# Performance work log

Measured on AMD Instinct MI355X. Metric: run time of the kernel, lower is better.

## Reference

```python
import jax, jax.numpy as jnp
import numpy as np

# Tsit5 Butcher tableau (Tsitouras 2011), 5th-order solution weights.
C2, C3, C4, C5 = 0.161, 0.327, 0.9, 0.9800255409045097
A21 = 0.161
A31, A32 = -0.008480655492356989, 0.335480655492357
A41, A42, A43 = 2.8971530571054935, -6.359448489975075, 4.3622954328695815
A51, A52, A53, A54 = 5.325864828439257, -11.748883564062828, 7.4955393428898365, -0.09249506636175525
A61, A62, A63, A64, A65 = 5.86145544294642, -12.92096931784711, 8.159367898576159, -0.071584973281401, -0.028269050394068383
B1, B2, B3, B4, B5, B6 = 0.09646076681806523, 0.01, 0.4798896504144996, 1.379008574103742, -3.290069515436081, 2.324710524099774


def setup_inputs() -> dict:
    key = jax.random.key(0)
    k0, k1, k2, k3 = jax.random.split(key, 4)
    B, D, W, T = 2048, 64, 128, 50
    y0 = jax.random.normal(k0, (B, D), dtype=jnp.float32)
    ts = (jnp.arange(T, dtype=jnp.float32)) * 0.02  # t0=0, t1=0.98, dt0=0.02
    # equinox-style MLP params (Linear stores weight as [out, in]); scaled for stability
    w0 = jax.random.normal(k1, (W, D + 1), dtype=jnp.float32) / np.sqrt(D + 1)
    b0 = jnp.zeros((W,), dtype=jnp.float32)
    w1 = jax.random.normal(k2, (W, W), dtype=jnp.float32) / np.sqrt(W)
    b1 = jnp.zeros((W,), dtype=jnp.float32)
    w2 = jax.random.normal(k3, (D, W), dtype=jnp.float32) / np.sqrt(W)
    b2 = jnp.zeros((D,), dtype=jnp.float32)
    return {"y0": y0, "ts": ts, "w0": w0, "b0": b0, "w1": w1, "b1": b1, "w2": w2, "b2": b2}


def reference(y0, ts, w0, b0, w1, b1, w2, b2):
    # dynamics f(t, y) = MLP(concat([t, y])), vectorized over batch
    def dyn(t, y):
        tcol = jnp.full((y.shape[0], 1), t, dtype=y.dtype)
        inp = jnp.concatenate([tcol, y], axis=1)           # [B, D+1]
        h = jax.nn.relu(inp @ w0.T + b0)                    # [B, W]
        h = jax.nn.relu(h @ w1.T + b1)                      # [B, W]
        return h @ w2.T + b2                                # [B, D]

    dt = ts[1] - ts[0]

    def step(y, t):
        k1 = dyn(t, y)
        k2 = dyn(t + C2 * dt, y + dt * (A21 * k1))
        k3 = dyn(t + C3 * dt, y + dt * (A31 * k1 + A32 * k2))
        k4 = dyn(t + C4 * dt, y + dt * (A41 * k1 + A42 * k2 + A43 * k3))
        k5 = dyn(t + C5 * dt, y + dt * (A51 * k1 + A52 * k2 + A53 * k3 + A54 * k4))
        k6 = dyn(t + dt, y + dt * (A61 * k1 + A62 * k2 + A63 * k3 + A64 * k4 + A65 * k5))
        y_new = y + dt * (B1 * k1 + B2 * k2 + B3 * k3 + B4 * k4 + B5 * k5 + B6 * k6)
        return y_new, None

    yT, _ = jax.lax.scan(step, y0, ts[:-1])  # 49 constant-size Tsit5 steps
    return yT
```

## Files before the change

kernel.cpp:

```cpp
#include <hip/hip_runtime.h>

typedef __attribute__((ext_vector_type(8))) short   short8;
typedef __attribute__((ext_vector_type(8))) __bf16  bf16x8;
typedef __attribute__((ext_vector_type(4))) __bf16  bf16x4;
typedef __attribute__((ext_vector_type(4))) float   f32x4;
typedef __attribute__((ext_vector_type(4))) unsigned short ushort4v;

#define NSTEPS 49

static __device__ __forceinline__ short8 as_s8(bf16x8 v) {
    return __builtin_bit_cast(short8, v);
}
static __device__ __forceinline__ bf16x4 pack4(f32x4 v) {
    bf16x4 b;
    b[0] = (__bf16)v[0]; b[1] = (__bf16)v[1];
    b[2] = (__bf16)v[2]; b[3] = (__bf16)v[3];
    return b;
}

#define MFMA(A, B, C) __builtin_amdgcn_mfma_f32_16x16x32_bf16((A), (B), (C), 0, 0, 0)

#define BUILD_XT(TV)                                                         \
    {                                                                        \
        bf16x8 v_;                                                           \
        _Pragma("unroll") for (int j_ = 0; j_ < 8; ++j_) v_[j_] = (__bf16)0.f; \
        if (q == 0) { v_[0] = (__bf16)(TV); v_[1] = (__bf16)1.0f; }          \
        xt = as_s8(v_);                                                      \
    }

#define RELU_PACK(AA, AB, OUT)                                               \
    {                                                                        \
        bf16x8 v_;                                                           \
        v_[0]=(__bf16)fmaxf((AA)[0],0.f); v_[1]=(__bf16)fmaxf((AA)[1],0.f);  \
        v_[2]=(__bf16)fmaxf((AA)[2],0.f); v_[3]=(__bf16)fmaxf((AA)[3],0.f);  \
        v_[4]=(__bf16)fmaxf((AB)[0],0.f); v_[5]=(__bf16)fmaxf((AB)[1],0.f);  \
        v_[6]=(__bf16)fmaxf((AB)[2],0.f); v_[7]=(__bf16)fmaxf((AB)[3],0.f);  \
        OUT = as_s8(v_);                                                     \
    }

#define STAGE(TN, HS)                                                        \
    {                                                                        \
        const f32x4 zz = {0.f, 0.f, 0.f, 0.f};                               \
                             \
        short8 xs0 = *(const short8*)(&XS[0][lane][0]);                      \
        short8 xs1 = *(const short8*)(&XS[1][lane][0]);                      \
        short8 xt; BUILD_XT(TN);                                             \
        f32x4 aA = MFMA(wL1[0], xs0, zz); aA = MFMA(wL1[1], xs1, aA);        \
        aA = MFMA(wL1[2], xt, aA);                                           \
        f32x4 aB = MFMA(wL1[3], xs0, zz); aB = MFMA(wL1[4], xs1, aB);        \
        aB = MFMA(wL1[5], xt, aB);                                           \
        short8 xhm; RELU_PACK(aA, aB, xhm);                                  \
        *(short8*)(&XH[w][lane][0]) = xhm;                                   \
        __syncthreads();                                                     \
                              \
        short8 xh0 = *(const short8*)(&XH[0][lane][0]);                      \
        short8 xh1 = *(const short8*)(&XH[1][lane][0]);                      \
        short8 xh2 = *(const short8*)(&XH[2][lane][0]);                      \
        short8 xh3 = *(const short8*)(&XH[3][lane][0]);                      \
        f32x4 gA = MFMA(wL2[0], xh0, bL2v[0]); gA = MFMA(wL2[1], xh1, gA);   \
        gA = MFMA(wL2[2], xh2, gA);            gA = MFMA(wL2[3], xh3, gA);   \
        f32x4 gB = MFMA(wL2[4], xh0, bL2v[1]); gB = MFMA(wL2[5], xh1, gB);   \
        gB = MFMA(wL2[6], xh2, gB);            gB = MFMA(wL2[7], xh3, gB);   \
        short8 xgm; RELU_PACK(gA, gB, xgm);                                  \
        *(short8*)(&XG[w][lane][0]) = xgm;                                   \
        __syncthreads();                                                     \
                    \
        short8 xg0 = *(const short8*)(&XG[0][lane][0]);                      \
        short8 xg1 = *(const short8*)(&XG[1][lane][0]);                      \
        short8 xg2 = *(const short8*)(&XG[2][lane][0]);                      \
        short8 xg3 = *(const short8*)(&XG[3][lane][0]);                      \
        kv = MFMA(wL3[0], xg0, bL3v); kv = MFMA(wL3[1], xg1, kv);            \
        kv = MFMA(wL3[2], xg2, kv);   kv = MFMA(wL3[3], xg3, kv);            \
        _Pragma("unroll")                                                    \
        for (int r_ = 0; r_ < 4; ++r_) si[r_] = pre[r_] + (HS) * kv[r_];     \
        *(ushort4v*)(&XS[w >> 1][lane][4 * (w & 1)]) =                       \
            __builtin_bit_cast(ushort4v, pack4(si));                        \
        __syncthreads();                                                     \
    }

extern "C" __global__ void __launch_bounds__(256, 1)
node_solve(const float* __restrict__ y0, const float* __restrict__ ts,
           const float* __restrict__ gw0, const float* __restrict__ gb0,
           const float* __restrict__ gw1, const float* __restrict__ gb1,
           const float* __restrict__ gw2, const float* __restrict__ gb2,
           float* __restrict__ out)
{
    __shared__ __align__(16) unsigned short XS[2][64][8];
    __shared__ __align__(16) unsigned short XH[4][64][8];
    __shared__ __align__(16) unsigned short XG[4][64][8];

    const int tid  = threadIdx.x;
    const int w    = tid >> 6;
    const int lane = tid & 63;
    const int q    = lane >> 4;
    const int c    = lane & 15;
    const int row0 = blockIdx.x << 4;

    short8 wL1[6];
    short8 wL2[8];
    short8 wL3[4];
    f32x4  bL2v[2], bL3v;

    #pragma unroll
    for (int p = 0; p < 2; ++p) {
        const int t = 2 * w + p;
        const int n = 16 * t + c;
        const float* w0r = gw0 + n * 65 + 1;
        #pragma unroll
        for (int ks = 0; ks < 2; ++ks) {
            bf16x8 v;
            #pragma unroll
            for (int j = 0; j < 8; ++j)
                v[j] = (__bf16)w0r[32*ks + 16*(j>>2) + 4*q + (j&3)];
            wL1[3*p + ks] = as_s8(v);
        }
        {
            bf16x8 v;
            #pragma unroll
            for (int j = 0; j < 8; ++j) v[j] = (__bf16)0.f;
            if (q == 0) { v[0] = (__bf16)gw0[n*65]; v[1] = (__bf16)gb0[n]; }
            wL1[3*p + 2] = as_s8(v);
        }
        const float* w1r = gw1 + n * 128;
        #pragma unroll
        for (int ks = 0; ks < 4; ++ks) {
            bf16x8 v;
            #pragma unroll
            for (int j = 0; j < 8; ++j)
                v[j] = (__bf16)w1r[32*ks + 16*(j>>2) + 4*q + (j&3)];
            wL2[4*p + ks] = as_s8(v);
        }
        bL2v[p] = *(const f32x4*)(gb1 + 16*t + 4*q);
    }
    {
        const int n = 16 * w + c;
        const float* w2r = gw2 + n * 128;
        #pragma unroll
        for (int ks = 0; ks < 4; ++ks) {
            bf16x8 v;
            #pragma unroll
            for (int j = 0; j < 8; ++j)
                v[j] = (__bf16)w2r[32*ks + 16*(j>>2) + 4*q + (j&3)];
            wL3[ks] = as_s8(v);
        }
        bL3v = *(const f32x4*)(gb2 + 16*w + 4*q);
    }

    f32x4 yn = *(const f32x4*)(y0 + (size_t)(row0 + c) * 64 + 16*w + 4*q);

    const float ts0 = ts[0];
    const float dtv = ts[1] - ts[0];

    const float e1 = dtv * 0.09646076681806523f, e2 = dtv * 0.01f;
    const float e3 = dtv * 0.4798896504144996f,  e4 = dtv * 1.379008574103742f;
    const float e5 = dtv * -3.290069515436081f,  e6 = dtv * 2.324710524099774f;
    const float h0 = dtv * 0.161f;
    const float h1 = dtv * 0.335480655492357f;
    const float h2 = dtv * 4.3622954328695815f;
    const float h3 = dtv * -0.09249506636175525f;
    const float h4 = dtv * -0.028269050394068383f;
    const float g31 = dtv * (-0.008480655492356989f - 0.09646076681806523f);
    const float g41 = dtv * (2.8971530571054935f    - 0.09646076681806523f);
    const float g42 = dtv * (-6.359448489975075f    - 0.01f);
    const float g51 = dtv * (5.325864828439257f     - 0.09646076681806523f);
    const float g52 = dtv * (-11.748883564062828f   - 0.01f);
    const float g53 = dtv * (7.4955393428898365f    - 0.4798896504144996f);
    const float g61 = dtv * (5.86145544294642f      - 0.09646076681806523f);
    const float g62 = dtv * (-12.92096931784711f    - 0.01f);
    const float g63 = dtv * (8.159367898576159f     - 0.4798896504144996f);
    const float g64 = dtv * (-0.071584973281401f    - 1.379008574103742f);

    *(ushort4v*)(&XS[w >> 1][lane][4 * (w & 1)]) =
        __builtin_bit_cast(ushort4v, pack4(yn));
    f32x4 pre = yn, si, kv;
    __syncthreads();

    #pragma unroll 1
    for (int step = 0; step < NSTEPS; ++step) {
        const float t0s = ts0 + (float)step * dtv;
        bf16x4 kb0, kb1, kb2, kb3;

        STAGE(t0s, h0)
        #pragma unroll
        for (int r = 0; r < 4; ++r) yn[r] += e1 * kv[r];
        kb0 = pack4(kv);
        #pragma unroll
        for (int r = 0; r < 4; ++r) pre[r] = yn[r] + g31 * (float)kb0[r];

        STAGE(t0s + 0.161f * dtv, h1)
        #pragma unroll
        for (int r = 0; r < 4; ++r) yn[r] += e2 * kv[r];
        kb1 = pack4(kv);
        #pragma unroll
        for (int r = 0; r < 4; ++r)
            pre[r] = yn[r] + g41 * (float)kb0[r] + g42 * (float)kb1[r];

        STAGE(t0s + 0.327f * dtv, h2)
        #pragma unroll
        for (int r = 0; r < 4; ++r) yn[r] += e3 * kv[r];
        kb2 = pack4(kv);
        #pragma unroll
        for (int r = 0; r < 4; ++r)
            pre[r] = yn[r] + g51 * (float)kb0[r] + g52 * (float)kb1[r]
                   + g53 * (float)kb2[r];

        STAGE(t0s + 0.9f * dtv, h3)
        #pragma unroll
        for (int r = 0; r < 4; ++r) yn[r] += e4 * kv[r];
        kb3 = pack4(kv);
        #pragma unroll
        for (int r = 0; r < 4; ++r)
            pre[r] = yn[r] + g61 * (float)kb0[r] + g62 * (float)kb1[r]
                   + g63 * (float)kb2[r] + g64 * (float)kb3[r];

        STAGE(t0s + 0.9800255409045097f * dtv, h4)
        #pragma unroll
        for (int r = 0; r < 4; ++r) { yn[r] += e5 * kv[r]; pre[r] = yn[r]; }

        STAGE(t0s + dtv, e6)
        #pragma unroll
        for (int r = 0; r < 4; ++r) { yn[r] = si[r]; pre[r] = si[r]; }
    }

    *(f32x4*)(&out[(size_t)(row0 + c) * 64 + 16*w + 4*q]) = yn;
}

extern "C" void kernel_launch(void* const* d_in, const int* in_sizes, int n_in,
                              void* d_out, int out_size, void* d_ws, size_t ws_size,
                              hipStream_t stream) {
    const float* y0 = (const float*)d_in[0];
    const float* ts = (const float*)d_in[1];
    const float* w0 = (const float*)d_in[2];
    const float* b0 = (const float*)d_in[3];
    const float* w1 = (const float*)d_in[4];
    const float* b1 = (const float*)d_in[5];
    const float* w2 = (const float*)d_in[6];
    const float* b2 = (const float*)d_in[7];
    float* out = (float*)d_out;

    node_solve<<<dim3(128), dim3(256), 0, stream>>>(y0, ts, w0, b0, w1, b1, w2, b2, out);
}
```

Before: 244.4 us.

## Process two 16-row batch tiles per block to interleave MFMA chains

Each block now handles 32 batch rows as two independent 16-row tiles, duplicating the shared-memory staging buffers and interleaving both tiles' MFMA chains within each stage. The intent is to hide MFMA and LDS latency in this serial, latency-bound solver and to amortize barriers and register-resident weights over more rows. In exchange the grid halves to 64 blocks, leaving more compute units idle, and register pressure per thread rises.

```diff
diff --git a/kernel.cpp b/kernel.cpp
--- a/kernel.cpp
+++ b/kernel.cpp
@@ -38,43 +38,72 @@
         OUT = as_s8(v_);                                                     \
     }
 
-#define STAGE(TN, HS)                                                        \
+#define STAGE2(TN, HS)                                                       \
     {                                                                        \
         const f32x4 zz = {0.f, 0.f, 0.f, 0.f};                               \
-                             \
-        short8 xs0 = *(const short8*)(&XS[0][lane][0]);                      \
-        short8 xs1 = *(const short8*)(&XS[1][lane][0]);                      \
         short8 xt; BUILD_XT(TN);                                             \
-        f32x4 aA = MFMA(wL1[0], xs0, zz); aA = MFMA(wL1[1], xs1, aA);        \
-        aA = MFMA(wL1[2], xt, aA);                                           \
-        f32x4 aB = MFMA(wL1[3], xs0, zz); aB = MFMA(wL1[4], xs1, aB);        \
-        aB = MFMA(wL1[5], xt, aB);                                           \
-        short8 xhm; RELU_PACK(aA, aB, xhm);                                  \
-        *(short8*)(&XH[w][lane][0]) = xhm;                                   \
+                 \
+        short8 xs0A = *(const short8*)(&XSA[0][lane][0]);                    \
+        short8 xs1A = *(const short8*)(&XSA[1][lane][0]);                    \
+        short8 xs0B = *(const short8*)(&XSB[0][lane][0]);                    \
+        short8 xs1B = *(const short8*)(&XSB[1][lane][0]);                    \
+        f32x4 hAa = MFMA(wL1[0], xs0A, zz); hAa = MFMA(wL1[1], xs1A, hAa);   \
+        hAa = MFMA(wL1[2], xt, hAa);                                         \
+        f32x4 hAb = MFMA(wL1[3], xs0A, zz); hAb = MFMA(wL1[4], xs1A, hAb);   \
+        hAb = MFMA(wL1[5], xt, hAb);                                         \
+        f32x4 hBa = MFMA(wL1[0], xs0B, zz); hBa = MFMA(wL1[1], xs1B, hBa);   \
+        hBa = MFMA(wL1[2], xt, hBa);                                         \
+        f32x4 hBb = MFMA(wL1[3], xs0B, zz); hBb = MFMA(wL1[4], xs1B, hBb);   \
+        hBb = MFMA(wL1[5], xt, hBb);                                         \
+        short8 xhmA; RELU_PACK(hAa, hAb, xhmA);                              \
+        short8 xhmB; RELU_PACK(hBa, hBb, xhmB);                              \
+        *(short8*)(&XHA[w][lane][0]) = xhmA;                                 \
+        *(short8*)(&XHB[w][lane][0]) = xhmB;                                 \
         __syncthreads();                                                     \
-                              \
-        short8 xh0 = *(const short8*)(&XH[0][lane][0]);                      \
-        short8 xh1 = *(const short8*)(&XH[1][lane][0]);                      \
-        short8 xh2 = *(const short8*)(&XH[2][lane][0]);                      \
-        short8 xh3 = *(const short8*)(&XH[3][lane][0]);                      \
-        f32x4 gA = MFMA(wL2[0], xh0, bL2v[0]); gA = MFMA(wL2[1], xh1, gA);   \
-        gA = MFMA(wL2[2], xh2, gA);            gA = MFMA(wL2[3], xh3, gA);   \
-        f32x4 gB = MFMA(wL2[4], xh0, bL2v[1]); gB = MFMA(wL2[5], xh1, gB);   \
-        gB = MFMA(wL2[6], xh2, gB);            gB = MFMA(wL2[7], xh3, gB);   \
-        short8 xgm; RELU_PACK(gA, gB, xgm);                                  \
-        *(short8*)(&XG[w][lane][0]) = xgm;                                   \
+                                              \
+        short8 xh0A = *(const short8*)(&XHA[0][lane][0]);                    \
+        short8 xh1A = *(const short8*)(&XHA[1][lane][0]);                    \
+        short8 xh2A = *(const short8*)(&XHA[2][lane][0]);                    \
+        short8 xh3A = *(const short8*)(&XHA[3][lane][0]);                    \
+        short8 xh0B = *(const short8*)(&XHB[0][lane][0]);                    \
+        short8 xh1B = *(const short8*)(&XHB[1][lane][0]);                    \
+        short8 xh2B = *(const short8*)(&XHB[2][lane][0]);                    \
+        short8 xh3B = *(const short8*)(&XHB[3][lane][0]);                    \
+        f32x4 gAa = MFMA(wL2[0], xh0A, bL2v[0]); gAa = MFMA(wL2[1], xh1A, gAa); \
+        gAa = MFMA(wL2[2], xh2A, gAa);           gAa = MFMA(wL2[3], xh3A, gAa); \
+        f32x4 gAb = MFMA(wL2[4], xh0A, bL2v[1]); gAb = MFMA(wL2[5], xh1A, gAb); \
+        gAb = MFMA(wL2[6], xh2A, gAb);           gAb = MFMA(wL2[7], xh3A, gAb); \
+        f32x4 gBa = MFMA(wL2[0], xh0B, bL2v[0]); gBa = MFMA(wL2[1], xh1B, gBa); \
+        gBa = MFMA(wL2[2], xh2B, gBa);           gBa = MFMA(wL2[3], xh3B, gBa); \
+        f32x4 gBb = MFMA(wL2[4], xh0B, bL2v[1]); gBb = MFMA(wL2[5], xh1B, gBb); \
+        gBb = MFMA(wL2[6], xh2B, gBb);           gBb = MFMA(wL2[7], xh3B, gBb); \
+        short8 xgmA; RELU_PACK(gAa, gAb, xgmA);                              \
+        short8 xgmB; RELU_PACK(gBa, gBb, xgmB);                              \
+        *(short8*)(&XGA[w][lane][0]) = xgmA;                                 \
+        *(short8*)(&XGB[w][lane][0]) = xgmB;                                 \
         __syncthreads();                                                     \
-                    \
-        short8 xg0 = *(const short8*)(&XG[0][lane][0]);                      \
-        short8 xg1 = *(const short8*)(&XG[1][lane][0]);                      \
-        short8 xg2 = *(const short8*)(&XG[2][lane][0]);                      \
-        short8 xg3 = *(const short8*)(&XG[3][lane][0]);                      \
-        kv = MFMA(wL3[0], xg0, bL3v); kv = MFMA(wL3[1], xg1, kv);            \
-        kv = MFMA(wL3[2], xg2, kv);   kv = MFMA(wL3[3], xg3, kv);            \
+                            \
+        short8 xg0A = *(const short8*)(&XGA[0][lane][0]);                    \
+        short8 xg1A = *(const short8*)(&XGA[1][lane][0]);                    \
+        short8 xg2A = *(const short8*)(&XGA[2][lane][0]);                    \
+        short8 xg3A = *(const short8*)(&XGA[3][lane][0]);                    \
+        short8 xg0B = *(const short8*)(&XGB[0][lane][0]);                    \
+        short8 xg1B = *(const short8*)(&XGB[1][lane][0]);                    \
+        short8 xg2B = *(const short8*)(&XGB[2][lane][0]);                    \
+        short8 xg3B = *(const short8*)(&XGB[3][lane][0]);                    \
+        kvA = MFMA(wL3[0], xg0A, bL3v); kvA = MFMA(wL3[1], xg1A, kvA);       \
+        kvA = MFMA(wL3[2], xg2A, kvA);  kvA = MFMA(wL3[3], xg3A, kvA);       \
+        kvB = MFMA(wL3[0], xg0B, bL3v); kvB = MFMA(wL3[1], xg1B, kvB);       \
+        kvB = MFMA(wL3[2], xg2B, kvB);  kvB = MFMA(wL3[3], xg3B, kvB);       \
         _Pragma("unroll")                                                    \
-        for (int r_ = 0; r_ < 4; ++r_) si[r_] = pre[r_] + (HS) * kv[r_];     \
-        *(ushort4v*)(&XS[w >> 1][lane][4 * (w & 1)]) =                       \
-            __builtin_bit_cast(ushort4v, pack4(si));                        \
+        for (int r_ = 0; r_ < 4; ++r_) {                                     \
+            siA[r_] = preA[r_] + (HS) * kvA[r_];                             \
+            siB[r_] = preB[r_] + (HS) * kvB[r_];                             \
+        }                                                                    \
+        *(ushort4v*)(&XSA[w >> 1][lane][4 * (w & 1)]) =                      \
+            __builtin_bit_cast(ushort4v, pack4(siA));                       \
+        *(ushort4v*)(&XSB[w >> 1][lane][4 * (w & 1)]) =                      \
+            __builtin_bit_cast(ushort4v, pack4(siB));                       \
         __syncthreads();                                                     \
     }
 
@@ -85,16 +114,16 @@
            const float* __restrict__ gw2, const float* __restrict__ gb2,
            float* __restrict__ out)
 {
-    __shared__ __align__(16) unsigned short XS[2][64][8];
-    __shared__ __align__(16) unsigned short XH[4][64][8];
-    __shared__ __align__(16) unsigned short XG[4][64][8];
+    __shared__ __align__(16) unsigned short XSA[2][64][8], XSB[2][64][8];
+    __shared__ __align__(16) unsigned short XHA[4][64][8], XHB[4][64][8];
+    __shared__ __align__(16) unsigned short XGA[4][64][8], XGB[4][64][8];
 
     const int tid  = threadIdx.x;
     const int w    = tid >> 6;
     const int lane = tid & 63;
     const int q    = lane >> 4;
     const int c    = lane & 15;
-    const int row0 = blockIdx.x << 4;
+    const int row0 = blockIdx.x << 5;
 
     short8 wL1[6];
     short8 wL2[8];
@@ -146,7 +175,8 @@
         bL3v = *(const f32x4*)(gb2 + 16*w + 4*q);
     }
 
-    f32x4 yn = *(const f32x4*)(y0 + (size_t)(row0 + c) * 64 + 16*w + 4*q);
+    f32x4 ynA = *(const f32x4*)(y0 + (size_t)(row0 + c)      * 64 + 16*w + 4*q);
+    f32x4 ynB = *(const f32x4*)(y0 + (size_t)(row0 + 16 + c) * 64 + 16*w + 4*q);
 
     const float ts0 = ts[0];
     const float dtv = ts[1] - ts[0];
@@ -170,59 +200,79 @@
     const float g63 = dtv * (8.159367898576159f     - 0.4798896504144996f);
     const float g64 = dtv * (-0.071584973281401f    - 1.379008574103742f);
 
-    *(ushort4v*)(&XS[w >> 1][lane][4 * (w & 1)]) =
-        __builtin_bit_cast(ushort4v, pack4(yn));
-    f32x4 pre = yn, si, kv;
+    *(ushort4v*)(&XSA[w >> 1][lane][4 * (w & 1)]) =
+        __builtin_bit_cast(ushort4v, pack4(ynA));
+    *(ushort4v*)(&XSB[w >> 1][lane][4 * (w & 1)]) =
+        __builtin_bit_cast(ushort4v, pack4(ynB));
+    f32x4 preA = ynA, preB = ynB, siA, siB, kvA, kvB;
     __syncthreads();
 
     #pragma unroll 1
     for (int step = 0; step < NSTEPS; ++step) {
         const float t0s = ts0 + (float)step * dtv;
-        bf16x4 kb0, kb1, kb2, kb3;
-
-        STAGE(t0s, h0)
-        #pragma unroll
-        for (int r = 0; r < 4; ++r) yn[r] += e1 * kv[r];
-        kb0 = pack4(kv);
-        #pragma unroll
-        for (int r = 0; r < 4; ++r) pre[r] = yn[r] + g31 * (float)kb0[r];
-
-        STAGE(t0s + 0.161f * dtv, h1)
-        #pragma unroll
-        for (int r = 0; r < 4; ++r) yn[r] += e2 * kv[r];
-        kb1 = pack4(kv);
-        #pragma unroll
-        for (int r = 0; r < 4; ++r)
-            pre[r] = yn[r] + g41 * (float)kb0[r] + g42 * (float)kb1[r];
-
-        STAGE(t0s + 0.327f * dtv, h2)
-        #pragma unroll
-        for (int r = 0; r < 4; ++r) yn[r] += e3 * kv[r];
-        kb2 = pack4(kv);
-        #pragma unroll
-        for (int r = 0; r < 4; ++r)
-            pre[r] = yn[r] + g51 * (float)kb0[r] + g52 * (float)kb1[r]
-                   + g53 * (float)kb2[r];
-
-        STAGE(t0s + 0.9f * dtv, h3)
-        #pragma unroll
-        for (int r = 0; r < 4; ++r) yn[r] += e4 * kv[r];
-        kb3 = pack4(kv);
-        #pragma unroll
-        for (int r = 0; r < 4; ++r)
-            pre[r] = yn[r] + g61 * (float)kb0[r] + g62 * (float)kb1[r]
-                   + g63 * (float)kb2[r] + g64 * (float)kb3[r];
-
-        STAGE(t0s + 0.9800255409045097f * dtv, h4)
-        #pragma unroll
-        for (int r = 0; r < 4; ++r) { yn[r] += e5 * kv[r]; pre[r] = yn[r]; }
-
-        STAGE(t0s + dtv, e6)
-        #pragma unroll
-        for (int r = 0; r < 4; ++r) { yn[r] = si[r]; pre[r] = si[r]; }
-    }
-
-    *(f32x4*)(&out[(size_t)(row0 + c) * 64 + 16*w + 4*q]) = yn;
+        bf16x4 kA0, kA1, kA2, kA3, kB0, kB1, kB2, kB3;
+
+        STAGE2(t0s, h0)
+        #pragma unroll
+        for (int r = 0; r < 4; ++r) { ynA[r] += e1 * kvA[r]; ynB[r] += e1 * kvB[r]; }
+        kA0 = pack4(kvA); kB0 = pack4(kvB);
+        #pragma unroll
+        for (int r = 0; r < 4; ++r) {
+            preA[r] = ynA[r] + g31 * (float)kA0[r];
+            preB[r] = ynB[r] + g31 * (float)kB0[r];
+        }
+
+        STAGE2(t0s + 0.161f * dtv, h1)
+        #pragma unroll
+        for (int r = 0; r < 4; ++r) { ynA[r] += e2 * kvA[r]; ynB[r] += e2 * kvB[r]; }
+        kA1 = pack4(kvA); kB1 = pack4(kvB);
+        #pragma unroll
+        for (int r = 0; r < 4; ++r) {
+            preA[r] = ynA[r] + g41 * (float)kA0[r] + g42 * (float)kA1[r];
+            preB[r] = ynB[r] + g41 * (float)kB0[r] + g42 * (float)kB1[r];
+        }
+
+        STAGE2(t0s + 0.327f * dtv, h2)
+        #pragma unroll
+        for (int r = 0; r < 4; ++r) { ynA[r] += e3 * kvA[r]; ynB[r] += e3 * kvB[r]; }
+        kA2 = pack4(kvA); kB2 = pack4(kvB);
+        #pragma unroll
+        for (int r = 0; r < 4; ++r) {
+            preA[r] = ynA[r] + g51 * (float)kA0[r] + g52 * (float)kA1[r]
+                    + g53 * (float)kA2[r];
+            preB[r] = ynB[r] + g51 * (float)kB0[r] + g52 * (float)kB1[r]
+                    + g53 * (float)kB2[r];
+        }
+
+        STAGE2(t0s + 0.9f * dtv, h3)
+        #pragma unroll
+        for (int r = 0; r < 4; ++r) { ynA[r] += e4 * kvA[r]; ynB[r] += e4 * kvB[r]; }
+        kA3 = pack4(kvA); kB3 = pack4(kvB);
+        #pragma unroll
+        for (int r = 0; r < 4; ++r) {
+            preA[r] = ynA[r] + g61 * (float)kA0[r] + g62 * (float)kA1[r]
+                    + g63 * (float)kA2[r] + g64 * (float)kA3[r];
+            preB[r] = ynB[r] + g61 * (float)kB0[r] + g62 * (float)kB1[r]
+                    + g63 * (float)kB2[r] + g64 * (float)kB3[r];
+        }
+
+        STAGE2(t0s + 0.9800255409045097f * dtv, h4)
+        #pragma unroll
+        for (int r = 0; r < 4; ++r) {
+            ynA[r] += e5 * kvA[r]; preA[r] = ynA[r];
+            ynB[r] += e5 * kvB[r]; preB[r] = ynB[r];
+        }
+
+        STAGE2(t0s + dtv, e6)
+        #pragma unroll
+        for (int r = 0; r < 4; ++r) {
+            ynA[r] = siA[r]; preA[r] = siA[r];
+            ynB[r] = siB[r]; preB[r] = siB[r];
+        }
+    }
+
+    *(f32x4*)(&out[(size_t)(row0 + c)      * 64 + 16*w + 4*q]) = ynA;
+    *(f32x4*)(&out[(size_t)(row0 + 16 + c) * 64 + 16*w + 4*q]) = ynB;
 }
 
 extern "C" void kernel_launch(void* const* d_in, const int* in_sizes, int n_in,
@@ -238,5 +288,5 @@
     const float* b2 = (const float*)d_in[7];
     float* out = (float*)d_out;
 
-    node_solve<<<dim3(128), dim3(256), 0, stream>>>(y0, ts, w0, b0, w1, b1, w2, b2, out);
-}
+    node_solve<<<dim3(64), dim3(256), 0, stream>>>(y0, ts, w0, b0, w1, b1, w2, b2, out);
+}
```

Result: slower. 345.5 us (+41.4%).

## Compute full layer-3 output redundantly per wave to drop state LDS exchange

Applied to the files above, without the earlier changes.

Each wave now computes all four 16-column tiles of the final layer instead of one, so every wave holds the full stage output in registers. The next stage's input fragments are built directly from those registers, which removes the XS shared buffer and one __syncthreads per stage. In exchange, layer-3 MFMA work is quadrupled per wave, register use grows (16 weight fragments, four-way state arrays), and the elementwise Runge-Kutta updates are replicated across waves.

```diff
diff --git a/kernel.cpp b/kernel.cpp
--- a/kernel.cpp
+++ b/kernel.cpp
@@ -2,23 +2,26 @@
 
 typedef __attribute__((ext_vector_type(8))) short   short8;
 typedef __attribute__((ext_vector_type(8))) __bf16  bf16x8;
-typedef __attribute__((ext_vector_type(4))) __bf16  bf16x4;
 typedef __attribute__((ext_vector_type(4))) float   f32x4;
-typedef __attribute__((ext_vector_type(4))) unsigned short ushort4v;
 
 #define NSTEPS 49
 
 static __device__ __forceinline__ short8 as_s8(bf16x8 v) {
     return __builtin_bit_cast(short8, v);
 }
-static __device__ __forceinline__ bf16x4 pack4(f32x4 v) {
-    bf16x4 b;
-    b[0] = (__bf16)v[0]; b[1] = (__bf16)v[1];
-    b[2] = (__bf16)v[2]; b[3] = (__bf16)v[3];
-    return b;
-}
 
 #define MFMA(A, B, C) __builtin_amdgcn_mfma_f32_16x16x32_bf16((A), (B), (C), 0, 0, 0)
+
+#define BUILD_XS(SRC)                                                        \
+    {                                                                        \
+        bf16x8 v0_, v1_;                                                     \
+        _Pragma("unroll")                                                    \
+        for (int j_ = 0; j_ < 8; ++j_) {                                     \
+            v0_[j_] = (__bf16)(SRC)[j_ >> 2][j_ & 3];                        \
+            v1_[j_] = (__bf16)(SRC)[(j_ >> 2) + 2][j_ & 3];                  \
+        }                                                                    \
+        xs0 = as_s8(v0_); xs1 = as_s8(v1_);                                  \
+    }
 
 #define BUILD_XT(TV)                                                         \
     {                                                                        \
@@ -27,6 +30,18 @@
         if (q == 0) { v_[0] = (__bf16)(TV); v_[1] = (__bf16)1.0f; }          \
         xt = as_s8(v_);                                                      \
     }
+
+#define STORE_KB(KB, KV)                                                     \
+    {                                                                        \
+        bf16x8 t0_, t1_;                                                     \
+        _Pragma("unroll")                                                    \
+        for (int j_ = 0; j_ < 8; ++j_) {                                     \
+            t0_[j_] = (__bf16)(KV)[j_ >> 2][j_ & 3];                         \
+            t1_[j_] = (__bf16)(KV)[(j_ >> 2) + 2][j_ & 3];                   \
+        }                                                                    \
+        (KB)[0] = t0_; (KB)[1] = t1_;                                        \
+    }
+#define KF(KB, V) ((float)(KB)[(V) >> 3][(V) & 7])
 
 #define RELU_PACK(AA, AB, OUT)                                               \
     {                                                                        \
@@ -41,10 +56,8 @@
 #define STAGE(TN, HS)                                                        \
     {                                                                        \
         const f32x4 zz = {0.f, 0.f, 0.f, 0.f};                               \
-                             \
-        short8 xs0 = *(const short8*)(&XS[0][lane][0]);                      \
-        short8 xs1 = *(const short8*)(&XS[1][lane][0]);                      \
         short8 xt; BUILD_XT(TN);                                             \
+                   \
         f32x4 aA = MFMA(wL1[0], xs0, zz); aA = MFMA(wL1[1], xs1, aA);        \
         aA = MFMA(wL1[2], xt, aA);                                           \
         f32x4 aB = MFMA(wL1[3], xs0, zz); aB = MFMA(wL1[4], xs1, aB);        \
@@ -52,7 +65,7 @@
         short8 xhm; RELU_PACK(aA, aB, xhm);                                  \
         *(short8*)(&XH[w][lane][0]) = xhm;                                   \
         __syncthreads();                                                     \
-                              \
+                                             \
         short8 xh0 = *(const short8*)(&XH[0][lane][0]);                      \
         short8 xh1 = *(const short8*)(&XH[1][lane][0]);                      \
         short8 xh2 = *(const short8*)(&XH[2][lane][0]);                      \
@@ -64,18 +77,25 @@
         short8 xgm; RELU_PACK(gA, gB, xgm);                                  \
         *(short8*)(&XG[w][lane][0]) = xgm;                                   \
         __syncthreads();                                                     \
-                    \
+                        \
         short8 xg0 = *(const short8*)(&XG[0][lane][0]);                      \
         short8 xg1 = *(const short8*)(&XG[1][lane][0]);                      \
         short8 xg2 = *(const short8*)(&XG[2][lane][0]);                      \
         short8 xg3 = *(const short8*)(&XG[3][lane][0]);                      \
-        kv = MFMA(wL3[0], xg0, bL3v); kv = MFMA(wL3[1], xg1, kv);            \
-        kv = MFMA(wL3[2], xg2, kv);   kv = MFMA(wL3[3], xg3, kv);            \
-        _Pragma("unroll")                                                    \
-        for (int r_ = 0; r_ < 4; ++r_) si[r_] = pre[r_] + (HS) * kv[r_];     \
-        *(ushort4v*)(&XS[w >> 1][lane][4 * (w & 1)]) =                       \
-            __builtin_bit_cast(ushort4v, pack4(si));                        \
-        __syncthreads();                                                     \
+        _Pragma("unroll")                                                    \
+        for (int t_ = 0; t_ < 4; ++t_) {                                     \
+            f32x4 ac_ = MFMA(wL3[4*t_ + 0], xg0, bL3v[t_]);                  \
+            ac_ = MFMA(wL3[4*t_ + 1], xg1, ac_);                             \
+            ac_ = MFMA(wL3[4*t_ + 2], xg2, ac_);                             \
+            ac_ = MFMA(wL3[4*t_ + 3], xg3, ac_);                             \
+            kv[t_] = ac_;                                                    \
+        }                                                                    \
+        f32x4 si_[4];                                                        \
+        _Pragma("unroll")                                                    \
+        for (int t_ = 0; t_ < 4; ++t_) si_[t_] = pre[t_] + (HS) * kv[t_];    \
+        BUILD_XS(si_);                                                       \
+        lastsi0 = si_[0]; lastsi1 = si_[1];                                  \
+        lastsi2 = si_[2]; lastsi3 = si_[3];                                  \
     }
 
 extern "C" __global__ void __launch_bounds__(256, 1)
@@ -85,7 +105,6 @@
            const float* __restrict__ gw2, const float* __restrict__ gb2,
            float* __restrict__ out)
 {
-    __shared__ __align__(16) unsigned short XS[2][64][8];
     __shared__ __align__(16) unsigned short XH[4][64][8];
     __shared__ __align__(16) unsigned short XG[4][64][8];
 
@@ -98,8 +117,8 @@
 
     short8 wL1[6];
     short8 wL2[8];
-    short8 wL3[4];
-    f32x4  bL2v[2], bL3v;
+    short8 wL3[16];
+    f32x4  bL2v[2], bL3v[4];
 
     #pragma unroll
     for (int p = 0; p < 2; ++p) {
@@ -132,8 +151,9 @@
         }
         bL2v[p] = *(const f32x4*)(gb1 + 16*t + 4*q);
     }
-    {
-        const int n = 16 * w + c;
+    #pragma unroll
+    for (int t = 0; t < 4; ++t) {
+        const int n = 16 * t + c;
         const float* w2r = gw2 + n * 128;
         #pragma unroll
         for (int ks = 0; ks < 4; ++ks) {
@@ -141,12 +161,15 @@
             #pragma unroll
             for (int j = 0; j < 8; ++j)
                 v[j] = (__bf16)w2r[32*ks + 16*(j>>2) + 4*q + (j&3)];
-            wL3[ks] = as_s8(v);
-        }
-        bL3v = *(const f32x4*)(gb2 + 16*w + 4*q);
-    }
-
-    f32x4 yn = *(const f32x4*)(y0 + (size_t)(row0 + c) * 64 + 16*w + 4*q);
+            wL3[4*t + ks] = as_s8(v);
+        }
+        bL3v[t] = *(const f32x4*)(gb2 + 16*t + 4*q);
+    }
+
+    f32x4 yn[4];
+    #pragma unroll
+    for (int t = 0; t < 4; ++t)
+        yn[t] = *(const f32x4*)(y0 + (size_t)(row0 + c) * 64 + 16*t + 4*q);
 
     const float ts0 = ts[0];
     const float dtv = ts[1] - ts[0];
@@ -170,59 +193,64 @@
     const float g63 = dtv * (8.159367898576159f     - 0.4798896504144996f);
     const float g64 = dtv * (-0.071584973281401f    - 1.379008574103742f);
 
-    *(ushort4v*)(&XS[w >> 1][lane][4 * (w & 1)]) =
-        __builtin_bit_cast(ushort4v, pack4(yn));
-    f32x4 pre = yn, si, kv;
-    __syncthreads();
+    short8 xs0, xs1;
+    f32x4  pre[4], kv[4];
+    f32x4  lastsi0, lastsi1, lastsi2, lastsi3;
+
+    BUILD_XS(yn);
+    #pragma unroll
+    for (int t = 0; t < 4; ++t) pre[t] = yn[t];
 
     #pragma unroll 1
     for (int step = 0; step < NSTEPS; ++step) {
         const float t0s = ts0 + (float)step * dtv;
-        bf16x4 kb0, kb1, kb2, kb3;
+        bf16x8 kb0[2], kb1[2], kb2[2], kb3[2];
 
         STAGE(t0s, h0)
         #pragma unroll
-        for (int r = 0; r < 4; ++r) yn[r] += e1 * kv[r];
-        kb0 = pack4(kv);
-        #pragma unroll
-        for (int r = 0; r < 4; ++r) pre[r] = yn[r] + g31 * (float)kb0[r];
+        for (int t = 0; t < 4; ++t) yn[t] += e1 * kv[t];
+        STORE_KB(kb0, kv);
+        #pragma unroll
+        for (int v = 0; v < 16; ++v)
+            pre[v>>2][v&3] = yn[v>>2][v&3] + g31 * KF(kb0, v);
 
         STAGE(t0s + 0.161f * dtv, h1)
         #pragma unroll
-        for (int r = 0; r < 4; ++r) yn[r] += e2 * kv[r];
-        kb1 = pack4(kv);
-        #pragma unroll
-        for (int r = 0; r < 4; ++r)
-            pre[r] = yn[r] + g41 * (float)kb0[r] + g42 * (float)kb1[r];
+        for (int t = 0; t < 4; ++t) yn[t] += e2 * kv[t];
+        STORE_KB(kb1, kv);
+        #pragma unroll
+        for (int v = 0; v < 16; ++v)
+            pre[v>>2][v&3] = yn[v>>2][v&3] + g41*KF(kb0,v) + g42*KF(kb1,v);
 
         STAGE(t0s + 0.327f * dtv, h2)
         #pragma unroll
-        for (int r = 0; r < 4; ++r) yn[r] += e3 * kv[r];
-        kb2 = pack4(kv);
-        #pragma unroll
-        for (int r = 0; r < 4; ++r)
-            pre[r] = yn[r] + g51 * (float)kb0[r] + g52 * (float)kb1[r]
-                   + g53 * (float)kb2[r];
+        for (int t = 0; t < 4; ++t) yn[t] += e3 * kv[t];
+        STORE_KB(kb2, kv);
+        #pragma unroll
+        for (int v = 0; v < 16; ++v)
+            pre[v>>2][v&3] = yn[v>>2][v&3] + g51*KF(kb0,v) + g52*KF(kb1,v)
+                           + g53*KF(kb2,v);
 
         STAGE(t0s + 0.9f * dtv, h3)
         #pragma unroll
-        for (int r = 0; r < 4; ++r) yn[r] += e4 * kv[r];
-        kb3 = pack4(kv);
-        #pragma unroll
-        for (int r = 0; r < 4; ++r)
-            pre[r] = yn[r] + g61 * (float)kb0[r] + g62 * (float)kb1[r]
-                   + g63 * (float)kb2[r] + g64 * (float)kb3[r];
+        for (int t = 0; t < 4; ++t) yn[t] += e4 * kv[t];
+        STORE_KB(kb3, kv);
+        #pragma unroll
+        for (int v = 0; v < 16; ++v)
+            pre[v>>2][v&3] = yn[v>>2][v&3] + g61*KF(kb0,v) + g62*KF(kb1,v)
+                           + g63*KF(kb2,v) + g64*KF(kb3,v);
 
         STAGE(t0s + 0.9800255409045097f * dtv, h4)
         #pragma unroll
-        for (int r = 0; r < 4; ++r) { yn[r] += e5 * kv[r]; pre[r] = yn[r]; }
+        for (int t = 0; t < 4; ++t) { yn[t] += e5 * kv[t]; pre[t] = yn[t]; }
 
         STAGE(t0s + dtv, e6)
-        #pragma unroll
-        for (int r = 0; r < 4; ++r) { yn[r] = si[r]; pre[r] = si[r]; }
-    }
-
-    *(f32x4*)(&out[(size_t)(row0 + c) * 64 + 16*w + 4*q]) = yn;
+        yn[0] = lastsi0; yn[1] = lastsi1; yn[2] = lastsi2; yn[3] = lastsi3;
+        #pragma unroll
+        for (int t = 0; t < 4; ++t) pre[t] = yn[t];
+    }
+
+    *(f32x4*)(&out[(size_t)(row0 + c) * 64 + 16*w + 4*q]) = yn[w];
 }
 
 extern "C" void kernel_launch(void* const* d_in, const int* in_sizes, int n_in,
```

Measured after the change: 277.4 us. +13.5%, slower.

## Compute full first layer redundantly per wave to drop one barrier per stage

Applied to the files above, without the earlier changes.

Each wave now holds all 24 first-layer weight fragments and computes the whole 128-wide hidden layer itself instead of a quarter slice, removing the XH shared buffer and one __syncthreads per stage. The state reads from shared memory move to the end of each stage. This spends four times the first-layer MFMA work and many more weight registers per wave in exchange for fewer barriers on a latency-bound serial chain.

```diff
diff --git a/kernel.cpp b/kernel.cpp
--- a/kernel.cpp
+++ b/kernel.cpp
@@ -41,30 +41,28 @@
 #define STAGE(TN, HS)                                                        \
     {                                                                        \
         const f32x4 zz = {0.f, 0.f, 0.f, 0.f};                               \
-                             \
-        short8 xs0 = *(const short8*)(&XS[0][lane][0]);                      \
-        short8 xs1 = *(const short8*)(&XS[1][lane][0]);                      \
         short8 xt; BUILD_XT(TN);                                             \
-        f32x4 aA = MFMA(wL1[0], xs0, zz); aA = MFMA(wL1[1], xs1, aA);        \
-        aA = MFMA(wL1[2], xt, aA);                                           \
-        f32x4 aB = MFMA(wL1[3], xs0, zz); aB = MFMA(wL1[4], xs1, aB);        \
-        aB = MFMA(wL1[5], xt, aB);                                           \
-        short8 xhm; RELU_PACK(aA, aB, xhm);                                  \
-        *(short8*)(&XH[w][lane][0]) = xhm;                                   \
-        __syncthreads();                                                     \
-                              \
-        short8 xh0 = *(const short8*)(&XH[0][lane][0]);                      \
-        short8 xh1 = *(const short8*)(&XH[1][lane][0]);                      \
-        short8 xh2 = *(const short8*)(&XH[2][lane][0]);                      \
-        short8 xh3 = *(const short8*)(&XH[3][lane][0]);                      \
-        f32x4 gA = MFMA(wL2[0], xh0, bL2v[0]); gA = MFMA(wL2[1], xh1, gA);   \
-        gA = MFMA(wL2[2], xh2, gA);            gA = MFMA(wL2[3], xh3, gA);   \
-        f32x4 gB = MFMA(wL2[4], xh0, bL2v[1]); gB = MFMA(wL2[5], xh1, gB);   \
-        gB = MFMA(wL2[6], xh2, gB);            gB = MFMA(wL2[7], xh3, gB);   \
+         \
+        short8 xh_[4];                                                       \
+        _Pragma("unroll")                                                    \
+        for (int p_ = 0; p_ < 4; ++p_) {                                     \
+            f32x4 aA_ = MFMA(wL1a[6*p_ + 0], xs0, zz);                       \
+            aA_ = MFMA(wL1a[6*p_ + 1], xs1, aA_);                            \
+            aA_ = MFMA(wL1a[6*p_ + 2], xt,  aA_);                            \
+            f32x4 aB_ = MFMA(wL1a[6*p_ + 3], xs0, zz);                       \
+            aB_ = MFMA(wL1a[6*p_ + 4], xs1, aB_);                            \
+            aB_ = MFMA(wL1a[6*p_ + 5], xt,  aB_);                            \
+            RELU_PACK(aA_, aB_, xh_[p_]);                                    \
+        }                                                                    \
+           \
+        f32x4 gA = MFMA(wL2[0], xh_[0], bL2v[0]); gA = MFMA(wL2[1], xh_[1], gA); \
+        gA = MFMA(wL2[2], xh_[2], gA);            gA = MFMA(wL2[3], xh_[3], gA); \
+        f32x4 gB = MFMA(wL2[4], xh_[0], bL2v[1]); gB = MFMA(wL2[5], xh_[1], gB); \
+        gB = MFMA(wL2[6], xh_[2], gB);            gB = MFMA(wL2[7], xh_[3], gB); \
         short8 xgm; RELU_PACK(gA, gB, xgm);                                  \
         *(short8*)(&XG[w][lane][0]) = xgm;                                   \
         __syncthreads();                                                     \
-                    \
+              \
         short8 xg0 = *(const short8*)(&XG[0][lane][0]);                      \
         short8 xg1 = *(const short8*)(&XG[1][lane][0]);                      \
         short8 xg2 = *(const short8*)(&XG[2][lane][0]);                      \
@@ -76,6 +74,9 @@
         *(ushort4v*)(&XS[w >> 1][lane][4 * (w & 1)]) =                       \
             __builtin_bit_cast(ushort4v, pack4(si));                        \
         __syncthreads();                                                     \
+            \
+        xs0 = *(const short8*)(&XS[0][lane][0]);                             \
+        xs1 = *(const short8*)(&XS[1][lane][0]);                             \
     }
 
 extern "C" __global__ void __launch_bounds__(256, 1)
@@ -86,7 +87,6 @@
            float* __restrict__ out)
 {
     __shared__ __align__(16) unsigned short XS[2][64][8];
-    __shared__ __align__(16) unsigned short XH[4][64][8];
     __shared__ __align__(16) unsigned short XG[4][64][8];
 
     const int tid  = threadIdx.x;
@@ -96,31 +96,35 @@
     const int c    = lane & 15;
     const int row0 = blockIdx.x << 4;
 
-    short8 wL1[6];
+    short8 wL1a[24];
     short8 wL2[8];
     short8 wL3[4];
     f32x4  bL2v[2], bL3v;
 
+    #pragma unroll
+    for (int t = 0; t < 8; ++t) {
+        const int n = 16 * t + c;
+        const float* w0r = gw0 + n * 65 + 1;
+        #pragma unroll
+        for (int ks = 0; ks < 2; ++ks) {
+            bf16x8 v;
+            #pragma unroll
+            for (int j = 0; j < 8; ++j)
+                v[j] = (__bf16)w0r[32*ks + 16*(j>>2) + 4*q + (j&3)];
+            wL1a[3*t + ks] = as_s8(v);
+        }
+        {
+            bf16x8 v;
+            #pragma unroll
+            for (int j = 0; j < 8; ++j) v[j] = (__bf16)0.f;
+            if (q == 0) { v[0] = (__bf16)gw0[n*65]; v[1] = (__bf16)gb0[n]; }
+            wL1a[3*t + 2] = as_s8(v);
+        }
+    }
     #pragma unroll
     for (int p = 0; p < 2; ++p) {
         const int t = 2 * w + p;
         const int n = 16 * t + c;
-        const float* w0r = gw0 + n * 65 + 1;
-        #pragma unroll
-        for (int ks = 0; ks < 2; ++ks) {
-            bf16x8 v;
-            #pragma unroll
-            for (int j = 0; j < 8; ++j)
-                v[j] = (__bf16)w0r[32*ks + 16*(j>>2) + 4*q + (j&3)];
-            wL1[3*p + ks] = as_s8(v);
-        }
-        {
-            bf16x8 v;
-            #pragma unroll
-            for (int j = 0; j < 8; ++j) v[j] = (__bf16)0.f;
-            if (q == 0) { v[0] = (__bf16)gw0[n*65]; v[1] = (__bf16)gb0[n]; }
-            wL1[3*p + 2] = as_s8(v);
-        }
         const float* w1r = gw1 + n * 128;
         #pragma unroll
         for (int ks = 0; ks < 4; ++ks) {
@@ -174,6 +178,8 @@
         __builtin_bit_cast(ushort4v, pack4(yn));
     f32x4 pre = yn, si, kv;
     __syncthreads();
+    short8 xs0 = *(const short8*)(&XS[0][lane][0]);
+    short8 xs1 = *(const short8*)(&XS[1][lane][0]);
 
     #pragma unroll 1
     for (int step = 0; step < NSTEPS; ++step) {
```

Result: slower. 281.9 us (+15.4%).
